# Kernel optimization log

Measured on AMD Instinct MI355X. Metric: run time of the kernel, lower is better.

The kernel has to match this reference:

```python
import jax, jax.numpy as jnp
import numpy as np

DIM = 256
N = 262144
LN_EPS = 1e-5


def setup_inputs() -> dict:
    key = jax.random.key(0)
    ks = jax.random.split(key, 16)
    d = DIM
    inp = {
        "x": jax.random.normal(ks[0], (N, d), dtype=jnp.float32),
        # main cell params (torch Linear stores weight as [out, in])
        "W_slow": jax.random.normal(ks[1], (d, d), dtype=jnp.float32) / np.sqrt(d),
        "V_slow": jax.random.normal(ks[2], (d, d), dtype=jnp.float32) * (0.1 / np.sqrt(d)),
        "gate_w": jax.random.normal(ks[3], (1, d), dtype=jnp.float32) / np.sqrt(d),
        "gate_b": jnp.zeros((1,), dtype=jnp.float32),
        # homeostatic core: Linear(4,16) -> LN(16) -> Tanh -> Linear(16,8) -> ReLU -> Linear(8,4) -> Sigmoid
        "sens1_w": jax.random.normal(ks[4], (16, 4), dtype=jnp.float32) * 0.5,
        "sens1_b": jnp.zeros((16,), dtype=jnp.float32),
        "ln_g": jnp.ones((16,), dtype=jnp.float32),
        "ln_b": jnp.zeros((16,), dtype=jnp.float32),
        "sens2_w": jax.random.normal(ks[5], (8, 16), dtype=jnp.float32) * 0.25,
        "sens2_b": jnp.zeros((8,), dtype=jnp.float32),
        "act_w": jax.random.normal(ks[6], (4, 8), dtype=jnp.float32) * 0.35,
        "act_b": jnp.zeros((4,), dtype=jnp.float32),
        # persistent Hebbian memory buffer
        "semantic_memory": jax.random.normal(ks[7], (d, d), dtype=jnp.float32) * 0.01,
    }
    return inp


def _homeostatic_controls(x, h_raw, w_norm, sens1_w, sens1_b, ln_g, ln_b,
                          sens2_w, sens2_b, act_w, act_b):
    # state vector: [surprise, excitation, fatigue, coherence]  -> [N, 4]
    surprise = jnp.abs(jnp.var(x, axis=1) - 0.5)          # unbiased=False variance
    excitation = jnp.mean(jnp.abs(h_raw), axis=1)
    fatigue = jnp.full_like(surprise, w_norm)
    coherence = jnp.full_like(surprise, 0.5)              # loss_val is None
    state = jnp.stack([surprise, excitation, fatigue, coherence], axis=1)
    z = state @ sens1_w.T + sens1_b                        # [N,16]
    mu = jnp.mean(z, axis=-1, keepdims=True)
    var = jnp.mean((z - mu) ** 2, axis=-1, keepdims=True)
    z = (z - mu) * jax.lax.rsqrt(var + LN_EPS) * ln_g + ln_b
    z = jnp.tanh(z)
    z = jax.nn.relu(z @ sens2_w.T + sens2_b)               # [N,8]
    controls = jax.nn.sigmoid(z @ act_w.T + act_b)         # [N,4]
    return controls


def reference(x, W_slow, V_slow, gate_w, gate_b,
              sens1_w, sens1_b, ln_g, ln_b, sens2_w, sens2_b, act_w, act_b,
              semantic_memory):
    # v = clamp(V_slow(x), -2, 2)
    v = jnp.clip(x @ V_slow.T, -2.0, 2.0)                  # [N, d]

    # homeostatic core (no_grad in torch)
    h_raw = x @ W_slow.T
    w_norm = jnp.linalg.norm(W_slow)
    controls = _homeostatic_controls(x, h_raw, w_norm, sens1_w, sens1_b,
                                     ln_g, ln_b, sens2_w, sens2_b, act_w, act_b)
    metabolic_rate = jnp.mean(controls[:, 0])
    gate_value = jnp.mean(controls[:, 2])

    gate = jax.nn.sigmoid(v @ gate_w.T + gate_b) * gate_value  # [N,1]
    output = jnp.clip(gate * v, -2.0, 2.0)

    # training-mode Hebbian memory update (no_grad in torch)
    batch = x.shape[0]
    hebb = (v.T @ x) / batch                               # [d, d]
    forget = jnp.mean(v ** 2, axis=0)[:, None] * semantic_memory
    delta = jnp.tanh(hebb - forget)
    mem = semantic_memory + delta * metabolic_rate * 0.1
    mem_norm = jnp.maximum(jnp.linalg.norm(mem), 1e-6)
    new_memory = mem / mem_norm * 0.5

    return output, new_memory
```

## Files before the change

### kernel.cpp

```cpp
#include <hip/hip_runtime.h>
#include <hip/hip_bf16.h>


#define NTOK 262144

typedef short s16x4 __attribute__((ext_vector_type(4)));
typedef short s16x8 __attribute__((ext_vector_type(8)));
typedef float f32x4 __attribute__((ext_vector_type(4)));
typedef unsigned int u32x4 __attribute__((ext_vector_type(4)));
typedef __bf16 bf16x8 __attribute__((ext_vector_type(8)));

static __device__ __forceinline__ float b2f(short s) {
  unsigned int u = ((unsigned int)(unsigned short)s) << 16;
  return __builtin_bit_cast(float, u);
}
static __device__ __forceinline__ short f2b(float f) {
  __hip_bfloat16 h = __float2bfloat16(f);
  return (short)__builtin_bit_cast(unsigned short, h);
}
static __device__ __forceinline__ float clip2(float f) {
  return fminf(2.f, fmaxf(-2.f, f));
}
static __device__ __forceinline__ unsigned int packu(short lo, short hi) {
  return (unsigned int)(unsigned short)lo | ((unsigned int)(unsigned short)hi << 16);
}
static __device__ __forceinline__ f32x4 mfma16(s16x8 a, s16x8 b, f32x4 c) {
  return __builtin_amdgcn_mfma_f32_16x16x32_bf16(
      __builtin_bit_cast(bf16x8, a), __builtin_bit_cast(bf16x8, b), c, 0, 0, 0);
}

__global__ __launch_bounds__(1024) void k_prep(const float* __restrict__ V,
                                               const float* __restrict__ W,
                                               short* __restrict__ Vf,
                                               short* __restrict__ Wf,
                                               float* __restrict__ scal) {
  int t = blockIdx.x * 1024 + threadIdx.x;
  int flat = t * 4;
  int col = flat >> 8, k0 = flat & 255;
  f32x4 v4 = *(const f32x4*)(V + flat);
  f32x4 w4 = *(const f32x4*)(W + flat);
  s16x4 vb, wb;
  float s = 0.f;
#pragma unroll
  for (int e = 0; e < 4; ++e) {
    vb[e] = f2b(v4[e]);
    wb[e] = f2b(w4[e]);
    s += w4[e] * w4[e];
  }
  int cb = col >> 4, lrr = col & 15;
  int ks = k0 >> 5, lgg = (k0 >> 3) & 3, j0 = k0 & 7;
  size_t g = (size_t)(((cb * 8 + ks) * 4 + lgg) * 16 + lrr) * 8 + j0;
  *(s16x4*)(Vf + g) = vb;
  *(s16x4*)(Wf + g) = wb;
#pragma unroll
  for (int d = 1; d < 64; d <<= 1) s += __shfl_xor(s, d);
  __shared__ float r[16];
  if ((threadIdx.x & 63) == 0) r[threadIdx.x >> 6] = s;
  __syncthreads();
  if (threadIdx.x == 0) {
    float tt = 0.f;
#pragma unroll
    for (int i = 0; i < 16; ++i) tt += r[i];
    atomicAdd(&scal[0], tt);
  }
}

__global__ __launch_bounds__(512) void k_main(
    const float* __restrict__ x, const short* __restrict__ Vf,
    const short* __restrict__ Wf, const float* __restrict__ gw,
    const float* __restrict__ gb, const float* __restrict__ s1w,
    const float* __restrict__ s1b, const float* __restrict__ lng,
    const float* __restrict__ lnb, const float* __restrict__ s2w,
    const float* __restrict__ s2b, const float* __restrict__ aw,
    const float* __restrict__ ab, short* __restrict__ v_out,
    float* __restrict__ g_out, float* __restrict__ scal) {
  __shared__ __align__(16) short xs[2][8192];
  __shared__ __align__(16) short vs[2][32 * 264];
  __shared__ float stat[4096];
  int tid = threadIdx.x;
  int lane = tid & 63, wid = tid >> 6;
  int lr = lane & 15, lg = lane >> 4;
  int np = tid >> 5, ic = tid & 31;
  int c0 = wid * 32;
  size_t n0 = (size_t)blockIdx.x * 1024;

#pragma unroll
  for (int q = 0; q < 4; ++q) stat[q * 512 + tid] = 0.f;

  float gw0 = gw[c0 + lr], gw1 = gw[c0 + 16 + lr];
  int sks = ic >> 2, slg = ic & 3;
  int rowa = 2 * np, rowb = 2 * np + 1;
  int sa = ((rowa >> 4) * 8 + sks) * 64 + ((slg * 16 + (rowa & 15)) ^ sks);
  int sb = ((rowb >> 4) * 8 + sks) * 64 + ((slg * 16 + (rowb & 15)) ^ sks);

  f32x4 rxa0, rxa1, rxb0, rxb1;

#define XLOAD(RB)                                              \
  {                                                            \
    const float* pa = x + (n0 + (RB) + rowa) * 256 + ic * 8;   \
    rxa0 = *(const f32x4*)pa;                                  \
    rxa1 = *(const f32x4*)(pa + 4);                            \
    rxb0 = *(const f32x4*)(pa + 256);                          \
    rxb1 = *(const f32x4*)(pa + 260);                          \
  }
#define CONV_STORE(BUF, RB)                                    \
  {                                                            \
    s16x8 ca, cb;                                              \
    float sA = 0.f, qA = 0.f, sB = 0.f, qB = 0.f;              \
    _Pragma("unroll") for (int j = 0; j < 4; ++j) {            \
      sA += rxa0[j] + rxa1[j];                                 \
      qA += rxa0[j] * rxa0[j] + rxa1[j] * rxa1[j];             \
      sB += rxb0[j] + rxb1[j];                                 \
      qB += rxb0[j] * rxb0[j] + rxb1[j] * rxb1[j];             \
      ca[j] = f2b(rxa0[j]); ca[4 + j] = f2b(rxa1[j]);          \
      cb[j] = f2b(rxb0[j]); cb[4 + j] = f2b(rxb1[j]);          \
    }                                                          \
    *(s16x8*)(xs[BUF] + sa * 8) = ca;                          \
    *(s16x8*)(xs[BUF] + sb * 8) = cb;                          \
    _Pragma("unroll") for (int d = 1; d < 32; d <<= 1) {       \
      sA += __shfl_xor(sA, d); qA += __shfl_xor(qA, d);        \
      sB += __shfl_xor(sB, d); qB += __shfl_xor(qB, d);        \
    }                                                          \
    if (ic == 0) {                                             \
      stat[2048 + (RB) + rowa] = sA;                           \
      stat[3072 + (RB) + rowa] = qA;                           \
      stat[2048 + (RB) + rowb] = sB;                           \
      stat[3072 + (RB) + rowb] = qB;                           \
    }                                                          \
  }

  XLOAD(0);
  CONV_STORE(0, 0);
  __syncthreads();

  for (int nt = 0; nt < 32; ++nt) {
    int buf = nt & 1;
    int rbase = nt * 32;
    if (nt > 0) {
      const short* vsp = vs[buf ^ 1];
#pragma unroll
      for (int q = 0; q < 2; ++q) {
        int item = q * 512 + tid;
        int row = item >> 5, c8 = item & 31;
        *(s16x8*)(v_out + (n0 + rbase - 32 + row) * 256 + c8 * 8) =
            *(const s16x8*)(vsp + row * 264 + c8 * 8);
      }
    }
    if (nt < 31) XLOAD(rbase + 32);
    f32x4 av[2][2] = {}, ah[2][2] = {};
    const short* xb = xs[buf];
#pragma unroll
    for (int ks = 0; ks < 8; ++ks) {
      s16x8 a0 = *(const s16x8*)(xb + ((ks * 64) + (lane ^ ks)) * 8);
      s16x8 a1 = *(const s16x8*)(xb + (((8 + ks) * 64) + (lane ^ ks)) * 8);
      s16x8 bv0 = *(const s16x8*)(Vf + (size_t)(((wid * 2 + 0) * 8 + ks) * 64 + lane) * 8);
      s16x8 bv1 = *(const s16x8*)(Vf + (size_t)(((wid * 2 + 1) * 8 + ks) * 64 + lane) * 8);
      s16x8 bw0 = *(const s16x8*)(Wf + (size_t)(((wid * 2 + 0) * 8 + ks) * 64 + lane) * 8);
      s16x8 bw1 = *(const s16x8*)(Wf + (size_t)(((wid * 2 + 1) * 8 + ks) * 64 + lane) * 8);
      av[0][0] = mfma16(a0, bv0, av[0][0]);
      av[0][1] = mfma16(a0, bv1, av[0][1]);
      av[1][0] = mfma16(a1, bv0, av[1][0]);
      av[1][1] = mfma16(a1, bv1, av[1][1]);
      ah[0][0] = mfma16(a0, bw0, ah[0][0]);
      ah[0][1] = mfma16(a0, bw1, ah[0][1]);
      ah[1][0] = mfma16(a1, bw0, ah[1][0]);
      ah[1][1] = mfma16(a1, bw1, ah[1][1]);
    }
#pragma unroll
    for (int mf = 0; mf < 2; ++mf)
#pragma unroll
      for (int e = 0; e < 4; ++e) {
        float v0 = clip2(av[mf][0][e]), v1 = clip2(av[mf][1][e]);
        av[mf][0][e] = v0; av[mf][1][e] = v1;
        float gd = v0 * gw0 + v1 * gw1;
        float hs = fabsf(ah[mf][0][e]) + fabsf(ah[mf][1][e]);
#pragma unroll
        for (int d = 1; d < 16; d <<= 1) {
          gd += __shfl_xor(gd, d);
          hs += __shfl_xor(hs, d);
        }
        if (lr == 0) {
          int row = rbase + mf * 16 + lg * 4 + e;
          atomicAdd(&stat[row], gd);
          atomicAdd(&stat[1024 + row], hs);
        }
      }
    {
      short* vsc = vs[buf];
#pragma unroll
      for (int mf = 0; mf < 2; ++mf)
#pragma unroll
        for (int nf = 0; nf < 2; ++nf)
#pragma unroll
          for (int e = 0; e < 4; ++e)
            vsc[(mf * 16 + lg * 4 + e) * 264 + c0 + nf * 16 + lr] =
                f2b(av[mf][nf][e]);
    }
    if (nt < 31) CONV_STORE(buf ^ 1, rbase + 32);
    __syncthreads();
  }
  {
    const short* vsp = vs[1];
#pragma unroll
    for (int q = 0; q < 2; ++q) {
      int item = q * 512 + tid;
      int row = item >> 5, c8 = item & 31;
      *(s16x8*)(v_out + (n0 + 992 + row) * 256 + c8 * 8) =
          *(const s16x8*)(vsp + row * 264 + c8 * 8);
    }
  }
#undef CONV_STORE
#undef XLOAD

  float c0s = 0.f, c2s = 0.f;
  float wnorm = sqrtf(scal[0]);
#pragma unroll
  for (int rr = 0; rr < 2; ++rr) {
    int r = tid + rr * 512;
    float mean = stat[2048 + r] * (1.f / 256.f);
    float var = stat[3072 + r] * (1.f / 256.f) - mean * mean;
    float st[4];
    st[0] = fabsf(var - 0.5f);
    st[1] = stat[1024 + r] * (1.f / 256.f);
    st[2] = wnorm;
    st[3] = 0.5f;
    float z[16];
#pragma unroll
    for (int o = 0; o < 16; ++o) {
      float a = s1b[o];
#pragma unroll
      for (int i = 0; i < 4; ++i) a += s1w[o * 4 + i] * st[i];
      z[o] = a;
    }
    float mu = 0.f;
#pragma unroll
    for (int o = 0; o < 16; ++o) mu += z[o];
    mu *= (1.f / 16.f);
    float vz = 0.f;
#pragma unroll
    for (int o = 0; o < 16; ++o) { float d2 = z[o] - mu; vz += d2 * d2; }
    vz *= (1.f / 16.f);
    float rs = rsqrtf(vz + 1e-5f);
#pragma unroll
    for (int o = 0; o < 16; ++o)
      z[o] = tanhf((z[o] - mu) * rs * lng[o] + lnb[o]);
    float z2[8];
#pragma unroll
    for (int o = 0; o < 8; ++o) {
      float a = s2b[o];
#pragma unroll
      for (int i = 0; i < 16; ++i) a += s2w[o * 16 + i] * z[i];
      z2[o] = fmaxf(a, 0.f);
    }
#pragma unroll
    for (int q = 0; q < 2; ++q) {
      int o = q * 2;
      float a = ab[o];
#pragma unroll
      for (int i = 0; i < 8; ++i) a += aw[o * 8 + i] * z2[i];
      float cc = 1.f / (1.f + expf(-a));
      if (q == 0) c0s += cc; else c2s += cc;
    }
    g_out[n0 + r] = 1.f / (1.f + expf(-(stat[r] + gb[0])));
  }
#pragma unroll
  for (int d = 1; d < 64; d <<= 1) {
    c0s += __shfl_xor(c0s, d);
    c2s += __shfl_xor(c2s, d);
  }
  if (lane == 0) {
    atomicAdd(&scal[1], c0s);
    atomicAdd(&scal[2], c2s);
  }
}

__global__ __launch_bounds__(512, 2) void k_hebb(
    const float* __restrict__ x, const short* __restrict__ v_in,
    const float* __restrict__ g_sig, const float* __restrict__ scal,
    float* __restrict__ colv2, float* __restrict__ parts,
    float* __restrict__ out0) {
  __shared__ __align__(16) unsigned int ldsT[2 * 256 * 17];
  unsigned int* vT = ldsT;
  unsigned int* xT = ldsT + 256 * 17;
  int tid = threadIdx.x;
  int lane = tid & 63, wid = tid >> 6;
  int lr = lane & 15, lg = lane >> 4;
  int wr = wid >> 2, wc = wid & 3;
  size_t n0 = (size_t)blockIdx.x * 1024;
  float gv = scal[2] * (1.f / 262144.f);

  f32x4 acc[8][4] = {};
  float cv2[8] = {0.f, 0.f, 0.f, 0.f, 0.f, 0.f, 0.f, 0.f};
  int np = tid >> 5, ic = tid & 31, i0 = ic * 8;

  for (int nt = 0; nt < 32; ++nt) {
    size_t nr = n0 + nt * 32 + np * 2;
    s16x8 va = *(const s16x8*)(v_in + nr * 256 + i0);
    s16x8 vb = *(const s16x8*)(v_in + (nr + 1) * 256 + i0);
    f32x4 xa0 = *(const f32x4*)(x + nr * 256 + i0);
    f32x4 xa1 = *(const f32x4*)(x + nr * 256 + i0 + 4);
    f32x4 xb0 = *(const f32x4*)(x + (nr + 1) * 256 + i0);
    f32x4 xb1 = *(const f32x4*)(x + (nr + 1) * 256 + i0 + 4);
    float sa = g_sig[nr] * gv, sb = g_sig[nr + 1] * gv;
    f32x4 oa0, oa1, ob0, ob1;
#pragma unroll
    for (int j = 0; j < 4; ++j) {
      float fa = b2f(va[j]), fA = b2f(va[4 + j]);
      float fb = b2f(vb[j]), fB = b2f(vb[4 + j]);
      cv2[j] += fa * fa + fb * fb;
      cv2[4 + j] += fA * fA + fB * fB;
      oa0[j] = clip2(fa * sa); oa1[j] = clip2(fA * sa);
      ob0[j] = clip2(fb * sb); ob1[j] = clip2(fB * sb);
      vT[(i0 + j) * 17 + np] = packu(va[j], vb[j]);
      vT[(i0 + 4 + j) * 17 + np] = packu(va[4 + j], vb[4 + j]);
      xT[(i0 + j) * 17 + np] = packu(f2b(xa0[j]), f2b(xb0[j]));
      xT[(i0 + 4 + j) * 17 + np] = packu(f2b(xa1[j]), f2b(xb1[j]));
    }
    *(f32x4*)(out0 + nr * 256 + i0) = oa0;
    *(f32x4*)(out0 + nr * 256 + i0 + 4) = oa1;
    *(f32x4*)(out0 + (nr + 1) * 256 + i0) = ob0;
    *(f32x4*)(out0 + (nr + 1) * 256 + i0 + 4) = ob1;
    __syncthreads();
    int npb = lg * 4;
    s16x8 bfr[4];
#pragma unroll
    for (int nf = 0; nf < 4; ++nf) {
      int j = wc * 64 + nf * 16 + lr;
      u32x4 q;
      q[0] = xT[j * 17 + npb]; q[1] = xT[j * 17 + npb + 1];
      q[2] = xT[j * 17 + npb + 2]; q[3] = xT[j * 17 + npb + 3];
      bfr[nf] = __builtin_bit_cast(s16x8, q);
    }
#pragma unroll
    for (int mf = 0; mf < 8; ++mf) {
      int i = wr * 128 + mf * 16 + lr;
      u32x4 q;
      q[0] = vT[i * 17 + npb]; q[1] = vT[i * 17 + npb + 1];
      q[2] = vT[i * 17 + npb + 2]; q[3] = vT[i * 17 + npb + 3];
      s16x8 afr = __builtin_bit_cast(s16x8, q);
#pragma unroll
      for (int nf = 0; nf < 4; ++nf)
        acc[mf][nf] = mfma16(afr, bfr[nf], acc[mf][nf]);
    }
    __syncthreads();
  }
  float* myp = parts + (size_t)blockIdx.x * 65536;
#pragma unroll
  for (int mf = 0; mf < 8; ++mf)
#pragma unroll
    for (int nf = 0; nf < 4; ++nf)
      *(f32x4*)(myp + (size_t)(((wid * 8 + mf) * 4 + nf) * 64 + lane) * 4) =
          acc[mf][nf];
  __syncthreads();
  float* cred = (float*)ldsT;
  if (tid < 256) cred[tid] = 0.f;
  __syncthreads();
#pragma unroll
  for (int j = 0; j < 8; ++j) atomicAdd(&cred[i0 + j], cv2[j]);
  __syncthreads();
  if (tid < 256) atomicAdd(&colv2[tid], cred[tid]);
}

__global__ __launch_bounds__(256) void k_mem1(
    const float* __restrict__ parts, const float* __restrict__ colv2,
    const float* __restrict__ sm, float* __restrict__ mem,
    float* __restrict__ scal) {
  int q = blockIdx.x * 256 + threadIdx.x;
  const float* src = parts + (size_t)q * 4;
  f32x4 acc = {0.f, 0.f, 0.f, 0.f};
#pragma unroll 4
  for (int p = 0; p < 256; ++p) acc += *(const f32x4*)(src + (size_t)p * 65536);
  int lane2 = q & 63, r = q >> 6;
  int lg = lane2 >> 4, lr = lane2 & 15;
  int nf = r & 3, mf = (r >> 2) & 7, wid = r >> 5;
  int wr = wid >> 2, wc = wid & 3;
  int j = wc * 64 + nf * 16 + lr;
  float mr = scal[1] * (1.f / 262144.f);
  float s = 0.f;
#pragma unroll
  for (int e = 0; e < 4; ++e) {
    int i = wr * 128 + mf * 16 + lg * 4 + e;
    float hebb = acc[e] * (1.f / 262144.f);
    float smv = sm[i * 256 + j];
    float forget = colv2[i] * (1.f / 262144.f) * smv;
    float m = smv + tanhf(hebb - forget) * mr * 0.1f;
    mem[i * 256 + j] = m;
    s += m * m;
  }
#pragma unroll
  for (int d = 1; d < 64; d <<= 1) s += __shfl_xor(s, d);
  __shared__ float r4[4];
  if ((threadIdx.x & 63) == 0) r4[threadIdx.x >> 6] = s;
  __syncthreads();
  if (threadIdx.x == 0) atomicAdd(&scal[3], r4[0] + r4[1] + r4[2] + r4[3]);
}

__global__ __launch_bounds__(256) void k_mem2(const float* __restrict__ mem,
                                              const float* __restrict__ scal,
                                              float* __restrict__ out1) {
  int idx = blockIdx.x * 256 + threadIdx.x;
  float scale = 0.5f / fmaxf(sqrtf(scal[3]), 1e-6f);
  out1[idx] = mem[idx] * scale;
}

extern "C" void kernel_launch(void* const* d_in, const int* in_sizes, int n_in,
                              void* d_out, int out_size, void* d_ws, size_t ws_size,
                              hipStream_t stream) {
  (void)in_sizes; (void)n_in; (void)out_size; (void)ws_size;
  const float* x   = (const float*)d_in[0];
  const float* Wm  = (const float*)d_in[1];
  const float* Vm  = (const float*)d_in[2];
  const float* gw  = (const float*)d_in[3];
  const float* gb  = (const float*)d_in[4];
  const float* s1w = (const float*)d_in[5];
  const float* s1b = (const float*)d_in[6];
  const float* lng = (const float*)d_in[7];
  const float* lnb = (const float*)d_in[8];
  const float* s2w = (const float*)d_in[9];
  const float* s2b = (const float*)d_in[10];
  const float* aw  = (const float*)d_in[11];
  const float* ab  = (const float*)d_in[12];
  const float* sm  = (const float*)d_in[13];
  float* out0 = (float*)d_out;
  float* out1 = out0 + (size_t)NTOK * 256;

  char* w = (char*)d_ws;
  short* v_ws  = (short*)w;
  float* g_ws  = (float*)(w + 134217728);
  float* scal  = (float*)(w + 135266304);
  float* colv2 = (float*)(w + 135266560);
  float* mem   = (float*)(w + 135267584);
  float* parts = (float*)(w + 135529728);
  short* Vf    = (short*)(w + 202638592);
  short* Wf    = (short*)(w + 202769664);

  hipMemsetAsync(scal, 0, 1280, stream);
  k_prep<<<16, 1024, 0, stream>>>(Vm, Wm, Vf, Wf, scal);
  k_main<<<256, 512, 0, stream>>>(x, Vf, Wf, gw, gb, s1w, s1b, lng, lnb,
                                  s2w, s2b, aw, ab, v_ws, g_ws, scal);
  k_hebb<<<256, 512, 0, stream>>>(x, v_ws, g_ws, scal, colv2, parts, out0);
  k_mem1<<<64, 256, 0, stream>>>(parts, colv2, sm, mem, scal);
  k_mem2<<<256, 256, 0, stream>>>(mem, scal, out1);
}
```

Baseline: 370.7 us.

## Split V and W matmuls across wave halves and store v directly to global

Waves 0-3 now compute the V projection and waves 4-7 the W projection, each over 64 columns, instead of every wave computing both over 32 columns. The LDS staging buffer for v is removed, and each lane writes its bf16 v values straight to global memory with scalar 2-byte stores. The launch bounds now request 4 blocks per SM. Together these aim to cut LDS usage and per-wave work to raise occupancy, at the cost of uncoalesced narrow global stores and idle W-waves during the v epilogue.

Result: slower. 547.9 us (+47.8%).

```diff
diff --git a/kernel.cpp b/kernel.cpp
--- a/kernel.cpp
+++ b/kernel.cpp
@@ -65,7 +65,7 @@
   }
 }
 
-__global__ __launch_bounds__(512) void k_main(
+__global__ __launch_bounds__(512, 4) void k_main(
     const float* __restrict__ x, const short* __restrict__ Vf,
     const short* __restrict__ Wf, const float* __restrict__ gw,
     const float* __restrict__ gb, const float* __restrict__ s1w,
@@ -75,19 +75,21 @@
     const float* __restrict__ ab, short* __restrict__ v_out,
     float* __restrict__ g_out, float* __restrict__ scal) {
   __shared__ __align__(16) short xs[2][8192];
-  __shared__ __align__(16) short vs[2][32 * 264];
   __shared__ float stat[4096];
   int tid = threadIdx.x;
   int lane = tid & 63, wid = tid >> 6;
   int lr = lane & 15, lg = lane >> 4;
+  int mat = wid >> 2, wc = wid & 3;
   int np = tid >> 5, ic = tid & 31;
-  int c0 = wid * 32;
   size_t n0 = (size_t)blockIdx.x * 1024;
 
 #pragma unroll
   for (int q = 0; q < 4; ++q) stat[q * 512 + tid] = 0.f;
 
-  float gw0 = gw[c0 + lr], gw1 = gw[c0 + 16 + lr];
+  const short* Bm = mat ? Wf : Vf;
+  float gw4[4];
+#pragma unroll
+  for (int nf = 0; nf < 4; ++nf) gw4[nf] = gw[wc * 64 + nf * 16 + lr];
   int sks = ic >> 2, slg = ic & 3;
   int rowa = 2 * np, rowb = 2 * np + 1;
   int sa = ((rowa >> 4) * 8 + sks) * 64 + ((slg * 16 + (rowa & 15)) ^ sks);
@@ -136,78 +138,63 @@
   for (int nt = 0; nt < 32; ++nt) {
     int buf = nt & 1;
     int rbase = nt * 32;
-    if (nt > 0) {
-      const short* vsp = vs[buf ^ 1];
-#pragma unroll
-      for (int q = 0; q < 2; ++q) {
-        int item = q * 512 + tid;
-        int row = item >> 5, c8 = item & 31;
-        *(s16x8*)(v_out + (n0 + rbase - 32 + row) * 256 + c8 * 8) =
-            *(const s16x8*)(vsp + row * 264 + c8 * 8);
-      }
-    }
     if (nt < 31) XLOAD(rbase + 32);
-    f32x4 av[2][2] = {}, ah[2][2] = {};
+    f32x4 acc[2][4] = {};
     const short* xb = xs[buf];
 #pragma unroll
     for (int ks = 0; ks < 8; ++ks) {
       s16x8 a0 = *(const s16x8*)(xb + ((ks * 64) + (lane ^ ks)) * 8);
       s16x8 a1 = *(const s16x8*)(xb + (((8 + ks) * 64) + (lane ^ ks)) * 8);
-      s16x8 bv0 = *(const s16x8*)(Vf + (size_t)(((wid * 2 + 0) * 8 + ks) * 64 + lane) * 8);
-      s16x8 bv1 = *(const s16x8*)(Vf + (size_t)(((wid * 2 + 1) * 8 + ks) * 64 + lane) * 8);
-      s16x8 bw0 = *(const s16x8*)(Wf + (size_t)(((wid * 2 + 0) * 8 + ks) * 64 + lane) * 8);
-      s16x8 bw1 = *(const s16x8*)(Wf + (size_t)(((wid * 2 + 1) * 8 + ks) * 64 + lane) * 8);
-      av[0][0] = mfma16(a0, bv0, av[0][0]);
-      av[0][1] = mfma16(a0, bv1, av[0][1]);
-      av[1][0] = mfma16(a1, bv0, av[1][0]);
-      av[1][1] = mfma16(a1, bv1, av[1][1]);
-      ah[0][0] = mfma16(a0, bw0, ah[0][0]);
-      ah[0][1] = mfma16(a0, bw1, ah[0][1]);
-      ah[1][0] = mfma16(a1, bw0, ah[1][0]);
-      ah[1][1] = mfma16(a1, bw1, ah[1][1]);
-    }
-#pragma unroll
-    for (int mf = 0; mf < 2; ++mf)
-#pragma unroll
-      for (int e = 0; e < 4; ++e) {
-        float v0 = clip2(av[mf][0][e]), v1 = clip2(av[mf][1][e]);
-        av[mf][0][e] = v0; av[mf][1][e] = v1;
-        float gd = v0 * gw0 + v1 * gw1;
-        float hs = fabsf(ah[mf][0][e]) + fabsf(ah[mf][1][e]);
-#pragma unroll
-        for (int d = 1; d < 16; d <<= 1) {
-          gd += __shfl_xor(gd, d);
-          hs += __shfl_xor(hs, d);
+#pragma unroll
+      for (int nf = 0; nf < 4; ++nf) {
+        s16x8 bf = *(const s16x8*)(
+            Bm + (size_t)((((wc * 4 + nf) * 8 + ks) * 64 + lane)) * 8);
+        acc[0][nf] = mfma16(a0, bf, acc[0][nf]);
+        acc[1][nf] = mfma16(a1, bf, acc[1][nf]);
+      }
+    }
+    if (mat == 0) {
+#pragma unroll
+      for (int mf = 0; mf < 2; ++mf)
+#pragma unroll
+        for (int e = 0; e < 4; ++e) {
+          float gd = 0.f;
+#pragma unroll
+          for (int nf = 0; nf < 4; ++nf) {
+            float v = clip2(acc[mf][nf][e]);
+            acc[mf][nf][e] = v;
+            gd += v * gw4[nf];
+          }
+#pragma unroll
+          for (int d = 1; d < 16; d <<= 1) gd += __shfl_xor(gd, d);
+          if (lr == 0) atomicAdd(&stat[rbase + mf * 16 + lg * 4 + e], gd);
         }
-        if (lr == 0) {
-          int row = rbase + mf * 16 + lg * 4 + e;
-          atomicAdd(&stat[row], gd);
-          atomicAdd(&stat[1024 + row], hs);
+#pragma unroll
+      for (int mf = 0; mf < 2; ++mf)
+#pragma unroll
+        for (int nf = 0; nf < 4; ++nf)
+#pragma unroll
+          for (int e = 0; e < 4; ++e) {
+            int row = rbase + mf * 16 + lg * 4 + e;
+            int col = wc * 64 + nf * 16 + lr;
+            v_out[(n0 + row) * 256 + col] = f2b(acc[mf][nf][e]);
+          }
+    } else {
+#pragma unroll
+      for (int mf = 0; mf < 2; ++mf)
+#pragma unroll
+        for (int e = 0; e < 4; ++e) {
+          float hs = 0.f;
+#pragma unroll
+          for (int nf = 0; nf < 4; ++nf) hs += fabsf(acc[mf][nf][e]);
+#pragma unroll
+          for (int d = 1; d < 16; d <<= 1) hs += __shfl_xor(hs, d);
+          if (lr == 0)
+            atomicAdd(&stat[1024 + rbase + mf * 16 + lg * 4 + e], hs);
         }
-      }
-    {
-      short* vsc = vs[buf];
-#pragma unroll
-      for (int mf = 0; mf < 2; ++mf)
-#pragma unroll
-        for (int nf = 0; nf < 2; ++nf)
-#pragma unroll
-          for (int e = 0; e < 4; ++e)
-            vsc[(mf * 16 + lg * 4 + e) * 264 + c0 + nf * 16 + lr] =
-                f2b(av[mf][nf][e]);
     }
     if (nt < 31) CONV_STORE(buf ^ 1, rbase + 32);
     __syncthreads();
-  }
-  {
-    const short* vsp = vs[1];
-#pragma unroll
-    for (int q = 0; q < 2; ++q) {
-      int item = q * 512 + tid;
-      int row = item >> 5, c8 = item & 31;
-      *(s16x8*)(v_out + (n0 + 992 + row) * 256 + c8 * 8) =
-          *(const s16x8*)(vsp + row * 264 + c8 * 8);
-    }
   }
 #undef CONV_STORE
 #undef XLOAD
```
